# Optimization experiments

Hardware: AMD Instinct MI355X
Metric: run time of the kernel (lower is better)

Reference implementation:

```python
import jax, jax.numpy as jnp
import numpy as np

B, C, IMG = 128, 3, 224
P = 16
NP = (IMG // P) ** 2          # 196 patches
S = 1 + NP                    # 197 tokens
D = 384
HEADS = 6
HD = D // HEADS               # 64
DEPTH = 12
HID = 4 * D                   # 1536
NCLS = 100
PATCH_DIM = C * P * P         # 768
EPS = 1e-5


def setup_inputs() -> dict:
    key = jax.random.key(0)
    ks = jax.random.split(key, 24)
    g = lambda k, shape, s=0.02: jax.random.normal(k, shape, dtype=jnp.float32) * s
    return {
        "x": jax.random.normal(ks[0], (B, C, IMG, IMG), dtype=jnp.float32),
        "patch_w": g(ks[1], (D, PATCH_DIM)),
        "patch_b": jnp.zeros((D,), jnp.float32),
        "cls_token": g(ks[2], (1, 1, D)),
        "pos_embed": g(ks[3], (1, S, D)),
        "ln1_g": jnp.ones((DEPTH, D), jnp.float32),
        "ln1_b": jnp.zeros((DEPTH, D), jnp.float32),
        "qkv_w": g(ks[4], (DEPTH, 3 * D, D)),
        "qkv_b": jnp.zeros((DEPTH, 3 * D), jnp.float32),
        "out_w": g(ks[5], (DEPTH, D, D)),
        "out_b": jnp.zeros((DEPTH, D), jnp.float32),
        "ln2_g": jnp.ones((DEPTH, D), jnp.float32),
        "ln2_b": jnp.zeros((DEPTH, D), jnp.float32),
        "fc1_w": g(ks[6], (DEPTH, HID, D)),
        "fc1_b": jnp.zeros((DEPTH, HID), jnp.float32),
        "fc2_w": g(ks[7], (DEPTH, D, HID)),
        "fc2_b": jnp.zeros((DEPTH, D), jnp.float32),
        "lnf_g": jnp.ones((D,), jnp.float32),
        "lnf_b": jnp.zeros((D,), jnp.float32),
        "head_w": g(ks[8], (NCLS, D)),
    }


def _ln(x, g, b):
    m = jnp.mean(x, axis=-1, keepdims=True)
    v = jnp.mean(jnp.square(x - m), axis=-1, keepdims=True)
    return (x - m) * jax.lax.rsqrt(v + EPS) * g + b


def reference(x, patch_w, patch_b, cls_token, pos_embed,
              ln1_g, ln1_b, qkv_w, qkv_b, out_w, out_b,
              ln2_g, ln2_b, fc1_w, fc1_b, fc2_w, fc2_b,
              lnf_g, lnf_b, head_w):
    b = x.shape[0]
    hp = IMG // P
    # patchify: unfold(2,P).unfold(3,P).permute(0,2,3,1,4,5) -> [B, N, C*P*P]
    patches = x.reshape(b, C, hp, P, hp, P).transpose(0, 2, 4, 1, 3, 5).reshape(b, NP, PATCH_DIM)
    tok = patches @ patch_w.T + patch_b                           # [B, NP, D]
    h = jnp.concatenate([jnp.broadcast_to(cls_token, (b, 1, D)), tok], axis=1)
    h = h + pos_embed[:, :S, :]
    scale = 1.0 / np.sqrt(HD).astype(np.float32)
    for i in range(DEPTH):
        xn = _ln(h, ln1_g[i], ln1_b[i])
        qkv = xn @ qkv_w[i].T + qkv_b[i]                          # [B, S, 3D]
        q, k, v = jnp.split(qkv, 3, axis=-1)
        q = q.reshape(b, S, HEADS, HD).transpose(0, 2, 1, 3) * scale
        k = k.reshape(b, S, HEADS, HD).transpose(0, 2, 1, 3)
        v = v.reshape(b, S, HEADS, HD).transpose(0, 2, 1, 3)
        attn = jax.nn.softmax(jnp.einsum('bhqd,bhkd->bhqk', q, k), axis=-1)
        ctx = jnp.einsum('bhqk,bhkd->bhqd', attn, v)
        ctx = ctx.transpose(0, 2, 1, 3).reshape(b, S, D)
        h = h + (ctx @ out_w[i].T + out_b[i])
        xn2 = _ln(h, ln2_g[i], ln2_b[i])
        hid = jax.nn.gelu(xn2 @ fc1_w[i].T + fc1_b[i], approximate=False)
        h = h + (hid @ fc2_w[i].T + fc2_b[i])
    cls = _ln(h[:, 0], lnf_g, lnf_b)
    return cls @ head_w.T                                         # [B, NCLS]
```

## Files before the change

kernel.cpp:

```cpp
#include <hip/hip_runtime.h>
#include <hip/hip_bf16.h>


#define S_ 197
#define D_ 384
#define BATCH 128

using bf16 = __hip_bfloat16;
typedef __attribute__((ext_vector_type(8))) __bf16 bf16x8;
typedef __attribute__((ext_vector_type(4))) float f32x4;

#if __has_builtin(__builtin_amdgcn_global_load_lds)
#define HAVE_GLL 1
__device__ __forceinline__ void gll16(const bf16* g, __bf16* l) {
  __builtin_amdgcn_global_load_lds(
      (const __attribute__((address_space(1))) void*)g,
      (__attribute__((address_space(3))) void*)l, 16, 0, 0);
}
#else
#define HAVE_GLL 0
#endif

__global__ __launch_bounds__(256) void k_f2b(const float* __restrict__ src,
                                             bf16* __restrict__ dst, int n4) {
  int i = blockIdx.x * 256 + threadIdx.x;
  if (i >= n4) return;
  float4 v = ((const float4*)src)[i];
  bf16 o[4] = {__float2bfloat16(v.x), __float2bfloat16(v.y),
               __float2bfloat16(v.z), __float2bfloat16(v.w)};
  ((uint2*)dst)[i] = *(uint2*)o;
}

__global__ __launch_bounds__(256) void k_embed_init(const float* __restrict__ cls,
                                                    const float* __restrict__ pos,
                                                    float* __restrict__ h) {
  int idx = blockIdx.x * 256 + threadIdx.x;
  if (idx >= BATCH * S_ * D_) return;
  int d = idx % D_;
  int s = (idx / D_) % S_;
  float v = pos[s * D_ + d];
  if (s == 0) v += cls[d];
  h[idx] = v;
}

__global__ __launch_bounds__(256) void k_patchify(const float* __restrict__ x,
                                                  bf16* __restrict__ patches) {
  int idx = blockIdx.x * 256 + threadIdx.x;
  if (idx >= BATCH * 196 * 768) return;
  int f = idx % 768;
  int n = (idx / 768) % 196;
  int b = idx / (768 * 196);
  int c = f >> 8, rem = f & 255, dy = rem >> 4, dx = rem & 15;
  int py = n / 14, px = n % 14;
  patches[idx] = __float2bfloat16(
      x[(((size_t)b * 3 + c) * 224 + py * 16 + dy) * 224 + px * 16 + dx]);
}

template <int MODE>
__global__ __launch_bounds__(256, 3) void k_gemm(const bf16* __restrict__ X,
                                                 const bf16* __restrict__ W,
                                                 const float* __restrict__ bias,
                                                 bf16* __restrict__ out,
                                                 float* __restrict__ res,
                                                 int N, int K, int remap) {
  __shared__ __align__(16) __bf16 As[128 * 32];
  __shared__ __align__(16) __bf16 Bs[128 * 32];
  const int tid = threadIdx.x;
  const int m0 = blockIdx.y * 128, n0 = blockIdx.x * 128;
  const int lane = tid & 63, w = tid >> 6;
  const int wr = w >> 1, wc = w & 1;
  const int l16 = lane & 15, quad = lane >> 4;
  f32x4 acc[4][4] = {};

  const int srow = w * 32 + (lane >> 2);
  const int scol = (lane & 3) * 8;
  const bf16* Ag = X + (size_t)(m0 + srow) * K + scol;
  const bf16* Bg = W + (size_t)(n0 + srow) * K + scol;
  __bf16* AsW = As + w * 32 * 32;
  __bf16* BsW = Bs + w * 32 * 32;

  for (int k0 = 0; k0 < K; k0 += 32) {
#if HAVE_GLL
    gll16(Ag + k0, AsW);
    gll16(Ag + k0 + (size_t)16 * K, AsW + 16 * 32);
    gll16(Bg + k0, BsW);
    gll16(Bg + k0 + (size_t)16 * K, BsW + 16 * 32);
#else
    *(uint4*)(AsW + (lane >> 2) * 32 + scol) = *(const uint4*)(Ag + k0);
    *(uint4*)(AsW + (16 + (lane >> 2)) * 32 + scol) = *(const uint4*)(Ag + k0 + (size_t)16 * K);
    *(uint4*)(BsW + (lane >> 2) * 32 + scol) = *(const uint4*)(Bg + k0);
    *(uint4*)(BsW + (16 + (lane >> 2)) * 32 + scol) = *(const uint4*)(Bg + k0 + (size_t)16 * K);
#endif
    __syncthreads();
    bf16x8 av[4], bv[4];
#pragma unroll
    for (int i = 0; i < 4; i++)
      av[i] = *(const bf16x8*)(&As[(wr * 64 + i * 16 + l16) * 32 + quad * 8]);
#pragma unroll
    for (int j = 0; j < 4; j++)
      bv[j] = *(const bf16x8*)(&Bs[(wc * 64 + j * 16 + l16) * 32 + quad * 8]);
#pragma unroll
    for (int i = 0; i < 4; i++)
#pragma unroll
      for (int j = 0; j < 4; j++)
        acc[i][j] = __builtin_amdgcn_mfma_f32_16x16x32_bf16(av[i], bv[j], acc[i][j], 0, 0, 0);
    __syncthreads();
  }

  float bvv[4];
#pragma unroll
  for (int j = 0; j < 4; j++)
    bvv[j] = bias[n0 + wc * 64 + j * 16 + l16];
#pragma unroll
  for (int i = 0; i < 4; i++) {
    const int rbase = m0 + wr * 64 + i * 16 + quad * 4;
#pragma unroll
    for (int j = 0; j < 4; j++) {
      const int col = n0 + wc * 64 + j * 16 + l16;
#pragma unroll
      for (int r = 0; r < 4; r++) {
        float v = acc[i][j][r] + bvv[j];
        int rw = rbase + r;
        if (MODE == 0) {
          out[(size_t)rw * N + col] = __float2bfloat16(v);
        } else if (MODE == 1) {
          float gl = 0.5f * v * (1.f + erff(v * 0.70710678118f));
          out[(size_t)rw * N + col] = __float2bfloat16(gl);
        } else {
          int hr = remap ? (rw + rw / 196 + 1) : rw;
          res[(size_t)hr * N + col] += v;
        }
      }
    }
  }
}

__global__ __launch_bounds__(128) void k_ln(const float* __restrict__ h,
                                            const float* __restrict__ g,
                                            const float* __restrict__ bt,
                                            bf16* __restrict__ xn) {
  const int r = blockIdx.x, t = threadIdx.x;
  const float* row = h + (size_t)r * D_;
  float x0 = row[t], x1 = row[t + 128], x2 = row[t + 256];
  float s = x0 + x1 + x2;
  float q = x0 * x0 + x1 * x1 + x2 * x2;
#pragma unroll
  for (int o = 32; o; o >>= 1) {
    s += __shfl_xor(s, o);
    q += __shfl_xor(q, o);
  }
  __shared__ float rs[2], rq[2];
  if ((t & 63) == 0) { rs[t >> 6] = s; rq[t >> 6] = q; }
  __syncthreads();
  s = rs[0] + rs[1];
  q = rq[0] + rq[1];
  const float mean = s * (1.f / 384.f);
  const float var = q * (1.f / 384.f) - mean * mean;
  const float rstd = rsqrtf(var + 1e-5f);
  bf16* o = xn + (size_t)r * D_;
  o[t] = __float2bfloat16((x0 - mean) * rstd * g[t] + bt[t]);
  o[t + 128] = __float2bfloat16((x1 - mean) * rstd * g[t + 128] + bt[t + 128]);
  o[t + 256] = __float2bfloat16((x2 - mean) * rstd * g[t + 256] + bt[t + 256]);
}

__global__ __launch_bounds__(256) void k_attn(const bf16* __restrict__ qkv,
                                              bf16* __restrict__ ctx) {
  const int bh = blockIdx.x;
  const int b = bh / 6, hd = bh % 6;
  const bf16* Qg = qkv + (size_t)b * S_ * 1152 + hd * 64;
  const bf16* Kg = Qg + 384;
  const bf16* Vg = Qg + 768;
  __shared__ __align__(16) __bf16 Vt[64 * 232];
  __shared__ __align__(16) __bf16 Ps[4][16 * 232];
  const int tid = threadIdx.x;
  const int lane = tid & 63, w = tid >> 6;
  const int l16 = lane & 15, quad = lane >> 4;
  const __bf16 z = (__bf16)0.0f;

  for (int i = tid; i < 64 * 35; i += 256) {
    int d = i / 35, k = 197 + i % 35;
    Vt[d * 232 + k] = z;
  }
  for (int i = tid; i < S_ * 64; i += 256) {
    int k = i >> 6, d = i & 63;
    Vt[d * 232 + k] = *(const __bf16*)&Vg[(size_t)k * 1152 + d];
  }
  for (int i = lane; i < 16 * 24; i += 64) {
    int r = i / 24, c = 208 + i % 24;
    Ps[w][r * 232 + c] = z;
  }
  __syncthreads();

  const bf16x8 zf = {};
  for (int band = w; band < 13; band += 4) {
    const int qrow = band * 16 + l16;
    bf16x8 aq0 = zf, aq1 = zf;
    if (qrow < S_) {
      aq0 = *(const bf16x8*)(Qg + (size_t)qrow * 1152 + quad * 8);
      aq1 = *(const bf16x8*)(Qg + (size_t)qrow * 1152 + 32 + quad * 8);
    }
    f32x4 sc[13];
#pragma unroll
    for (int t = 0; t < 13; t++) {
      const int krow = t * 16 + l16;
      bf16x8 bk0 = zf, bk1 = zf;
      if (krow < S_) {
        bk0 = *(const bf16x8*)(Kg + (size_t)krow * 1152 + quad * 8);
        bk1 = *(const bf16x8*)(Kg + (size_t)krow * 1152 + 32 + quad * 8);
      }
      f32x4 a = {};
      a = __builtin_amdgcn_mfma_f32_16x16x32_bf16(aq0, bk0, a, 0, 0, 0);
      a = __builtin_amdgcn_mfma_f32_16x16x32_bf16(aq1, bk1, a, 0, 0, 0);
      sc[t] = a;
    }
#pragma unroll
    for (int t = 0; t < 13; t++)
#pragma unroll
      for (int r = 0; r < 4; r++) sc[t][r] *= 0.125f;
    if (l16 >= 5) {
#pragma unroll
      for (int r = 0; r < 4; r++) sc[12][r] = -1e30f;
    }
    f32x4 mx = sc[0];
#pragma unroll
    for (int t = 1; t < 13; t++)
#pragma unroll
      for (int r = 0; r < 4; r++) mx[r] = fmaxf(mx[r], sc[t][r]);
#pragma unroll
    for (int o = 1; o < 16; o <<= 1)
#pragma unroll
      for (int r = 0; r < 4; r++) mx[r] = fmaxf(mx[r], __shfl_xor(mx[r], o));
    f32x4 sum = {};
#pragma unroll
    for (int t = 0; t < 13; t++)
#pragma unroll
      for (int r = 0; r < 4; r++) {
        float p = __expf(sc[t][r] - mx[r]);
        sc[t][r] = p;
        sum[r] += p;
      }
#pragma unroll
    for (int o = 1; o < 16; o <<= 1)
#pragma unroll
      for (int r = 0; r < 4; r++) sum[r] += __shfl_xor(sum[r], o);
    f32x4 rinv;
#pragma unroll
    for (int r = 0; r < 4; r++) rinv[r] = 1.0f / sum[r];
#pragma unroll
    for (int t = 0; t < 13; t++)
#pragma unroll
      for (int r = 0; r < 4; r++)
        Ps[w][(quad * 4 + r) * 232 + t * 16 + l16] = (__bf16)sc[t][r];
    f32x4 oacc[4] = {};
#pragma unroll
    for (int ks = 0; ks < 7; ks++) {
      bf16x8 pa = *(const bf16x8*)&Ps[w][l16 * 232 + ks * 32 + quad * 8];
#pragma unroll
      for (int c = 0; c < 4; c++) {
        bf16x8 bv = *(const bf16x8*)&Vt[(c * 16 + l16) * 232 + ks * 32 + quad * 8];
        oacc[c] = __builtin_amdgcn_mfma_f32_16x16x32_bf16(pa, bv, oacc[c], 0, 0, 0);
      }
    }
    const int orow = band * 16 + quad * 4;
#pragma unroll
    for (int c = 0; c < 4; c++)
#pragma unroll
      for (int r = 0; r < 4; r++) {
        const int rw = orow + r;
        if (rw < S_)
          ctx[((size_t)b * S_ + rw) * D_ + hd * 64 + c * 16 + l16] =
              __float2bfloat16(oacc[c][r] * rinv[r]);
      }
  }
}

__global__ __launch_bounds__(128) void k_head(const float* __restrict__ h,
                                              const float* __restrict__ g,
                                              const float* __restrict__ bt,
                                              const float* __restrict__ hw,
                                              float* __restrict__ out) {
  const int b = blockIdx.x, t = threadIdx.x;
  const float* row = h + (size_t)b * S_ * D_;
  float x0 = row[t], x1 = row[t + 128], x2 = row[t + 256];
  float s = x0 + x1 + x2;
  float q = x0 * x0 + x1 * x1 + x2 * x2;
#pragma unroll
  for (int o = 32; o; o >>= 1) {
    s += __shfl_xor(s, o);
    q += __shfl_xor(q, o);
  }
  __shared__ float rs[2], rq[2];
  if ((t & 63) == 0) { rs[t >> 6] = s; rq[t >> 6] = q; }
  __syncthreads();
  s = rs[0] + rs[1];
  q = rq[0] + rq[1];
  const float mean = s * (1.f / 384.f);
  const float var = q * (1.f / 384.f) - mean * mean;
  const float rstd = rsqrtf(var + 1e-5f);
  __shared__ float clsn[384];
  clsn[t] = (x0 - mean) * rstd * g[t] + bt[t];
  clsn[t + 128] = (x1 - mean) * rstd * g[t + 128] + bt[t + 128];
  clsn[t + 256] = (x2 - mean) * rstd * g[t + 256] + bt[t + 256];
  __syncthreads();
  if (t < 100) {
    const float* wr = hw + (size_t)t * D_;
    float a = 0.f;
    for (int d = 0; d < 384; d++) a += clsn[d] * wr[d];
    out[b * 100 + t] = a;
  }
}

extern "C" void kernel_launch(void* const* d_in, const int* in_sizes, int n_in,
                              void* d_out, int out_size, void* d_ws, size_t ws_size,
                              hipStream_t stream) {
  (void)in_sizes; (void)n_in; (void)out_size; (void)ws_size;
  const float* x       = (const float*)d_in[0];
  const float* patch_w = (const float*)d_in[1];
  const float* patch_b = (const float*)d_in[2];
  const float* cls_tok = (const float*)d_in[3];
  const float* pos_emb = (const float*)d_in[4];
  const float* ln1_g   = (const float*)d_in[5];
  const float* ln1_b   = (const float*)d_in[6];
  const float* qkv_w   = (const float*)d_in[7];
  const float* qkv_b   = (const float*)d_in[8];
  const float* out_w   = (const float*)d_in[9];
  const float* out_b   = (const float*)d_in[10];
  const float* ln2_g   = (const float*)d_in[11];
  const float* ln2_b   = (const float*)d_in[12];
  const float* fc1_w   = (const float*)d_in[13];
  const float* fc1_b   = (const float*)d_in[14];
  const float* fc2_w   = (const float*)d_in[15];
  const float* fc2_b   = (const float*)d_in[16];
  const float* lnf_g   = (const float*)d_in[17];
  const float* lnf_b   = (const float*)d_in[18];
  const float* head_w  = (const float*)d_in[19];
  float* out = (float*)d_out;

  const size_t R = (size_t)BATCH * S_;
  char* p = (char*)d_ws;
  float* h  = (float*)p; p += R * 384 * 4;
  bf16* xn  = (bf16*)p;  p += R * 384 * 2;
  bf16* u   = (bf16*)p;  p += R * 1536 * 2;
  bf16* qkvb = u;
  bf16* ctxb = u + R * 1152;
  bf16* hidb = u;
  bf16* patches = u;
  bf16* wb  = (bf16*)p;
  bf16* patch_wb = wb;
  bf16* qkv_wb   = patch_wb + 294912;
  bf16* out_wb   = qkv_wb + 5308416;
  bf16* fc1_wb   = out_wb + 1769472;
  bf16* fc2_wb   = fc1_wb + 7077888;

  k_f2b<<<dim3((294912 / 4 + 255) / 256), dim3(256), 0, stream>>>(patch_w, patch_wb, 294912 / 4);
  k_f2b<<<dim3((5308416 / 4 + 255) / 256), dim3(256), 0, stream>>>(qkv_w, qkv_wb, 5308416 / 4);
  k_f2b<<<dim3((1769472 / 4 + 255) / 256), dim3(256), 0, stream>>>(out_w, out_wb, 1769472 / 4);
  k_f2b<<<dim3((7077888 / 4 + 255) / 256), dim3(256), 0, stream>>>(fc1_w, fc1_wb, 7077888 / 4);
  k_f2b<<<dim3((7077888 / 4 + 255) / 256), dim3(256), 0, stream>>>(fc2_w, fc2_wb, 7077888 / 4);

  k_embed_init<<<dim3((BATCH * S_ * D_) / 256), dim3(256), 0, stream>>>(cls_tok, pos_emb, h);
  k_patchify<<<dim3((BATCH * 196 * 768) / 256), dim3(256), 0, stream>>>(x, patches);
  k_gemm<2><<<dim3(3, 196), dim3(256), 0, stream>>>(patches, patch_wb, patch_b, nullptr, h, 384, 768, 1);

  for (int i = 0; i < 12; i++) {
    k_ln<<<dim3((unsigned)R), dim3(128), 0, stream>>>(h, ln1_g + i * 384, ln1_b + i * 384, xn);
    k_gemm<0><<<dim3(9, 197), dim3(256), 0, stream>>>(xn, qkv_wb + (size_t)i * 1152 * 384,
                                                      qkv_b + i * 1152, qkvb, nullptr, 1152, 384, 0);
    k_attn<<<dim3(768), dim3(256), 0, stream>>>(qkvb, ctxb);
    k_gemm<2><<<dim3(3, 197), dim3(256), 0, stream>>>(ctxb, out_wb + (size_t)i * 384 * 384,
                                                      out_b + i * 384, nullptr, h, 384, 384, 0);
    k_ln<<<dim3((unsigned)R), dim3(128), 0, stream>>>(h, ln2_g + i * 384, ln2_b + i * 384, xn);
    k_gemm<1><<<dim3(12, 197), dim3(256), 0, stream>>>(xn, fc1_wb + (size_t)i * 1536 * 384,
                                                       fc1_b + i * 1536, hidb, nullptr, 1536, 384, 0);
    k_gemm<2><<<dim3(3, 197), dim3(256), 0, stream>>>(hidb, fc2_wb + (size_t)i * 384 * 1536,
                                                      fc2_b + i * 384, nullptr, h, 384, 1536, 0);
  }
  k_head<<<dim3(128), dim3(128), 0, stream>>>(h, lnf_g, lnf_b, head_w, out);
}
```

Before: 3.706 ms.

## Double-buffer GEMM LDS tiles with XOR swizzle and raise occupancy hint

The bf16 MFMA GEMM now keeps two LDS buffers per operand and prefetches the next K-slice while computing on the current one. This cuts the loop to one barrier per iteration and overlaps global-to-LDS loads with MFMA work. An XOR swizzle on the 16-byte column chunks, applied on the global read side and undone on the LDS read, is meant to reduce LDS bank conflicts. The launch-bounds occupancy hint rises from 3 to 4 blocks, while LDS use per block doubles to 32 KB, which adds register and LDS pressure.

Result: no change. 3.700 ms (-0.2%).

```diff
diff --git a/kernel.cpp b/kernel.cpp
--- a/kernel.cpp
+++ b/kernel.cpp
@@ -57,14 +57,14 @@
 }
 
 template <int MODE>
-__global__ __launch_bounds__(256, 3) void k_gemm(const bf16* __restrict__ X,
+__global__ __launch_bounds__(256, 4) void k_gemm(const bf16* __restrict__ X,
                                                  const bf16* __restrict__ W,
                                                  const float* __restrict__ bias,
                                                  bf16* __restrict__ out,
                                                  float* __restrict__ res,
                                                  int N, int K, int remap) {
-  __shared__ __align__(16) __bf16 As[128 * 32];
-  __shared__ __align__(16) __bf16 Bs[128 * 32];
+  __shared__ __align__(16) __bf16 As[2][128 * 32];
+  __shared__ __align__(16) __bf16 Bs[2][128 * 32];
   const int tid = threadIdx.x;
   const int m0 = blockIdx.y * 128, n0 = blockIdx.x * 128;
   const int lane = tid & 63, w = tid >> 6;
@@ -73,32 +73,49 @@
   f32x4 acc[4][4] = {};
 
   const int srow = w * 32 + (lane >> 2);
-  const int scol = (lane & 3) * 8;
+  const int scol = (((lane & 3) ^ ((lane >> 3) & 3)) << 3);
   const bf16* Ag = X + (size_t)(m0 + srow) * K + scol;
   const bf16* Bg = W + (size_t)(n0 + srow) * K + scol;
-  __bf16* AsW = As + w * 32 * 32;
-  __bf16* BsW = Bs + w * 32 * 32;
-
+  const int ldsW = w * 32 * 32;
+
+  const int jx8 = ((quad ^ ((l16 >> 1) & 3)) << 3);
+  const int aoff = (wr * 64 + l16) * 32 + jx8;
+  const int boff = (wc * 64 + l16) * 32 + jx8;
+
+#if HAVE_GLL
+#define STAGE(buf, k0)                                         \
+  do {                                                         \
+    gll16(Ag + (k0), &As[buf][ldsW]);                          \
+    gll16(Ag + (k0) + (size_t)16 * K, &As[buf][ldsW + 512]);   \
+    gll16(Bg + (k0), &Bs[buf][ldsW]);                          \
+    gll16(Bg + (k0) + (size_t)16 * K, &Bs[buf][ldsW + 512]);   \
+  } while (0)
+#else
+#define STAGE(buf, k0)                                                        \
+  do {                                                                        \
+    *(uint4*)(&As[buf][ldsW + (lane >> 2) * 32 + (lane & 3) * 8]) =           \
+        *(const uint4*)(Ag + (k0));                                           \
+    *(uint4*)(&As[buf][ldsW + 512 + (lane >> 2) * 32 + (lane & 3) * 8]) =     \
+        *(const uint4*)(Ag + (k0) + (size_t)16 * K);                          \
+    *(uint4*)(&Bs[buf][ldsW + (lane >> 2) * 32 + (lane & 3) * 8]) =           \
+        *(const uint4*)(Bg + (k0));                                           \
+    *(uint4*)(&Bs[buf][ldsW + 512 + (lane >> 2) * 32 + (lane & 3) * 8]) =     \
+        *(const uint4*)(Bg + (k0) + (size_t)16 * K);                          \
+  } while (0)
+#endif
+
+  STAGE(0, 0);
+  __syncthreads();
   for (int k0 = 0; k0 < K; k0 += 32) {
-#if HAVE_GLL
-    gll16(Ag + k0, AsW);
-    gll16(Ag + k0 + (size_t)16 * K, AsW + 16 * 32);
-    gll16(Bg + k0, BsW);
-    gll16(Bg + k0 + (size_t)16 * K, BsW + 16 * 32);
-#else
-    *(uint4*)(AsW + (lane >> 2) * 32 + scol) = *(const uint4*)(Ag + k0);
-    *(uint4*)(AsW + (16 + (lane >> 2)) * 32 + scol) = *(const uint4*)(Ag + k0 + (size_t)16 * K);
-    *(uint4*)(BsW + (lane >> 2) * 32 + scol) = *(const uint4*)(Bg + k0);
-    *(uint4*)(BsW + (16 + (lane >> 2)) * 32 + scol) = *(const uint4*)(Bg + k0 + (size_t)16 * K);
-#endif
-    __syncthreads();
+    const int cb = (k0 >> 5) & 1;
+    if (k0 + 32 < K) STAGE(cb ^ 1, k0 + 32);
     bf16x8 av[4], bv[4];
 #pragma unroll
     for (int i = 0; i < 4; i++)
-      av[i] = *(const bf16x8*)(&As[(wr * 64 + i * 16 + l16) * 32 + quad * 8]);
+      av[i] = *(const bf16x8*)(&As[cb][aoff + i * 512]);
 #pragma unroll
     for (int j = 0; j < 4; j++)
-      bv[j] = *(const bf16x8*)(&Bs[(wc * 64 + j * 16 + l16) * 32 + quad * 8]);
+      bv[j] = *(const bf16x8*)(&Bs[cb][boff + j * 512]);
 #pragma unroll
     for (int i = 0; i < 4; i++)
 #pragma unroll
@@ -106,6 +123,7 @@
         acc[i][j] = __builtin_amdgcn_mfma_f32_16x16x32_bf16(av[i], bv[j], acc[i][j], 0, 0, 0);
     __syncthreads();
   }
+#undef STAGE
 
   float bvv[4];
 #pragma unroll
```
